# Kernel tuning notes

Hardware: AMD Instinct MI355X
Metric: run time of the kernel (lower is better)

Reference implementation:

```python
import jax, jax.numpy as jnp
import numpy as np

N_NODES = 50000
N_EDGES = 800000
D = 96
DEPTH = 2


def setup_inputs() -> dict:
    key = jax.random.key(0)
    ks = jax.random.split(key, 8)
    scale = 1.0 / np.sqrt(D)
    x = jax.random.normal(ks[0], (N_NODES, D), dtype=jnp.float32)
    W0 = jax.random.normal(ks[1], (DEPTH, D, D), dtype=jnp.float32) * scale
    b0 = jnp.zeros((DEPTH, D), dtype=jnp.float32)
    W1 = jax.random.normal(ks[2], (DEPTH, D, D), dtype=jnp.float32) * scale
    b1 = jnp.zeros((DEPTH, D), dtype=jnp.float32)
    W2 = jax.random.normal(ks[3], (DEPTH, 2 * D, D), dtype=jnp.float32) * (1.0 / np.sqrt(2 * D))
    b2 = jnp.zeros((DEPTH, D), dtype=jnp.float32)
    edge_src = jax.random.randint(ks[4], (N_EDGES,), 0, N_NODES, dtype=jnp.int64 if jax.config.jax_enable_x64 else jnp.int32)
    edge_dst = jnp.sort(jax.random.randint(ks[5], (N_EDGES,), 0, N_NODES, dtype=jnp.int64 if jax.config.jax_enable_x64 else jnp.int32))
    return {"x": x, "W0": W0, "b0": b0, "W1": W1, "b1": b1,
            "W2": W2, "b2": b2, "edge_src": edge_src, "edge_dst": edge_dst}


def reference(x, W0, b0, W1, b1, W2, b2, edge_src, edge_dst):
    # x: [N, D] node features; edge lists define sparse adjacency A (A[dst, src] = 1).
    n = x.shape[0]
    depth = W0.shape[0]
    for i in range(depth):
        h_self = x @ W1[i] + b1[i]                      # [N, D] self transform
        h_nb = x @ W0[i] + b0[i]                        # [N, D] neighbor transform
        # sparse.mm(A, h_nb): sum of h_nb over in-neighbors of each vertex
        agg = jax.ops.segment_sum(h_nb[edge_src], edge_dst, num_segments=n)  # [N, D]
        x = jnp.concatenate([h_self, agg], axis=-1) @ W2[i] + b2[i]          # [N, D]
        # torch.std uses unbiased estimator (ddof=1)
        x = x / jnp.std(x, axis=-1, ddof=1, keepdims=True)
    return x
```

## Files before the change

kernel.cpp:

```cpp
#include <hip/hip_runtime.h>
#include <hip/hip_bf16.h>

typedef __attribute__((ext_vector_type(8))) short short8;
typedef __attribute__((ext_vector_type(16))) float f32x16;

__device__ __forceinline__ float bf2f(unsigned short h){
  union{unsigned u; float f;} c; c.u = ((unsigned)h)<<16; return c.f;
}
__device__ __forceinline__ unsigned short f2bf(float f){
  union{float f; unsigned u;} c; c.f = f;
  return (unsigned short)((c.u + 0x7fffu + ((c.u>>16)&1u))>>16);
}


__global__ void k_wcb(const float* __restrict__ W0, const float* __restrict__ W1,
                      const float* __restrict__ W2, const float* __restrict__ b0,
                      const float* __restrict__ b1, const float* __restrict__ b2,
                      unsigned short* __restrict__ WcF, float* __restrict__ cvec,
                      float* __restrict__ dvec, int depth){
  int b = blockIdx.x, c = threadIdx.x;
  int nwc = depth*192;
  if (b < nwc){
    int i = b/192, k = b%192;
    const float* w  = (k<96) ? (W1 + (size_t)i*96*96 + (size_t)k*96)
                             : (W0 + (size_t)i*96*96 + (size_t)(k-96)*96);
    const float* w2 = W2 + (size_t)i*192*96 + (k<96 ? 0 : 96*96);
    float s0=0.f,s1=0.f,s2=0.f,s3=0.f;
    for (int j=0;j<96;j+=4){
      s0 += w[j]   * w2[(j)*96 + c];
      s1 += w[j+1] * w2[(j+1)*96 + c];
      s2 += w[j+2] * w2[(j+2)*96 + c];
      s3 += w[j+3] * w2[(j+3)*96 + c];
    }
    float s = (s0+s1)+(s2+s3);
    int kt = k>>4, hfk=(k>>3)&1, jj=k&7;
    int t=c>>5, cl=c&31;
    WcF[(size_t)((i*12+kt)*3+t)*512 + (size_t)(hfk*32+cl)*8 + jj] = f2bf(s);
  } else {
    int i = b - nwc;
    const float* w2 = W2 + (size_t)i*192*96;
    float s = b2[i*96+c], d=0.f;
    for (int j=0;j<96;++j){
      s += b1[i*96+j]*w2[j*96+c];
      d += b0[i*96+j]*w2[(96+j)*96+c];
    }
    cvec[i*96+c]=s; dvec[i*96+c]=d;
  }
}

__global__ __launch_bounds__(256) void k_prep(
    const float* __restrict__ x, unsigned short* __restrict__ xb,
    unsigned short* __restrict__ xf, const int* __restrict__ dst, int nE,
    int* __restrict__ rs, int nN, int castBlocks){
  if ((int)blockIdx.x < castBlocks){
    int tid = blockIdx.x*256 + threadIdx.x;
    if (tid >= nN*12) return;
    int n = tid/12, q = tid%12;
    const float4* src = reinterpret_cast<const float4*>(x + (size_t)n*96 + q*8);
    float4 f0 = src[0], f1 = src[1];
    uint4 o;
    o.x = (unsigned)f2bf(f0.x) | ((unsigned)f2bf(f0.y)<<16);
    o.y = (unsigned)f2bf(f0.z) | ((unsigned)f2bf(f0.w)<<16);
    o.z = (unsigned)f2bf(f1.x) | ((unsigned)f2bf(f1.y)<<16);
    o.w = (unsigned)f2bf(f1.z) | ((unsigned)f2bf(f1.w)<<16);
    *reinterpret_cast<uint4*>(xb + (size_t)n*96 + q*8) = o;
    int strip=n>>5, cl=n&31, kt=q>>1, hf=q&1;
    *reinterpret_cast<uint4*>(xf + ((size_t)(strip*6+kt)*64 + hf*32+cl)*8) = o;
  } else {
    int n = ((int)blockIdx.x - castBlocks)*256 + threadIdx.x;
    if (n > nN) return;
    int lo=0, hi=nE;
    while(lo<hi){int mid=(lo+hi)>>1; if(dst[mid]<n) lo=mid+1; else hi=mid;}
    rs[n]=lo;
  }
}

__global__ __launch_bounds__(256) void k_frag(
    const unsigned short* __restrict__ xb, unsigned short* __restrict__ xf, int nN){
  int tid = blockIdx.x*256+threadIdx.x;
  if (tid >= nN*12) return;
  int n=tid/12, q=tid%12;
  uint4 v = *reinterpret_cast<const uint4*>(xb + (size_t)n*96 + q*8);
  int strip=n>>5, cl=n&31, kt=q>>1, hf=q&1;
  *reinterpret_cast<uint4*>(xf + ((size_t)(strip*6+kt)*64 + hf*32+cl)*8) = v;
}

__device__ __forceinline__ void acc8(float* a, uint4 v){
  a[0] += bf2f((unsigned short)(v.x & 0xffffu));
  a[1] += bf2f((unsigned short)(v.x >> 16));
  a[2] += bf2f((unsigned short)(v.y & 0xffffu));
  a[3] += bf2f((unsigned short)(v.y >> 16));
  a[4] += bf2f((unsigned short)(v.z & 0xffffu));
  a[5] += bf2f((unsigned short)(v.z >> 16));
  a[6] += bf2f((unsigned short)(v.w & 0xffffu));
  a[7] += bf2f((unsigned short)(v.w >> 16));
}

__global__ __launch_bounds__(192) void k_agg(
    const unsigned short* __restrict__ xb, const int* __restrict__ esrc,
    const int* __restrict__ rs, unsigned short* __restrict__ xaf,
    int* __restrict__ deg, int nN)
{
  int n = blockIdx.x*16 + threadIdx.y;
  if (n >= nN) return;
  const int q = threadIdx.x;
  const unsigned short* xq = xb + q*8;
  const int e0 = rs[n], e1 = rs[n+1];
  if (q == 0) deg[n] = e1 - e0;

  float a[8] = {0,0,0,0,0,0,0,0};

  int e = e0;
  for (; e+8 <= e1; e += 8){
    int s0 = esrc[e],   s1 = esrc[e+1], s2 = esrc[e+2], s3 = esrc[e+3];
    int s4 = esrc[e+4], s5 = esrc[e+5], s6 = esrc[e+6], s7 = esrc[e+7];
    uint4 v0 = *reinterpret_cast<const uint4*>(xq + (size_t)s0*96);
    uint4 v1 = *reinterpret_cast<const uint4*>(xq + (size_t)s1*96);
    uint4 v2 = *reinterpret_cast<const uint4*>(xq + (size_t)s2*96);
    uint4 v3 = *reinterpret_cast<const uint4*>(xq + (size_t)s3*96);
    uint4 v4 = *reinterpret_cast<const uint4*>(xq + (size_t)s4*96);
    uint4 v5 = *reinterpret_cast<const uint4*>(xq + (size_t)s5*96);
    uint4 v6 = *reinterpret_cast<const uint4*>(xq + (size_t)s6*96);
    uint4 v7 = *reinterpret_cast<const uint4*>(xq + (size_t)s7*96);
    acc8(a, v0); acc8(a, v1); acc8(a, v2); acc8(a, v3);
    acc8(a, v4); acc8(a, v5); acc8(a, v6); acc8(a, v7);
  }
  for (; e+4 <= e1; e += 4){
    int s0 = esrc[e], s1 = esrc[e+1], s2 = esrc[e+2], s3 = esrc[e+3];
    uint4 v0 = *reinterpret_cast<const uint4*>(xq + (size_t)s0*96);
    uint4 v1 = *reinterpret_cast<const uint4*>(xq + (size_t)s1*96);
    uint4 v2 = *reinterpret_cast<const uint4*>(xq + (size_t)s2*96);
    uint4 v3 = *reinterpret_cast<const uint4*>(xq + (size_t)s3*96);
    acc8(a, v0); acc8(a, v1); acc8(a, v2); acc8(a, v3);
  }
  for (; e < e1; ++e){
    int s = esrc[e];
    uint4 v = *reinterpret_cast<const uint4*>(xq + (size_t)s*96);
    acc8(a, v);
  }

  uint4 o;
  o.x = (unsigned)f2bf(a[0]) | ((unsigned)f2bf(a[1]) << 16);
  o.y = (unsigned)f2bf(a[2]) | ((unsigned)f2bf(a[3]) << 16);
  o.z = (unsigned)f2bf(a[4]) | ((unsigned)f2bf(a[5]) << 16);
  o.w = (unsigned)f2bf(a[6]) | ((unsigned)f2bf(a[7]) << 16);
  int strip=n>>5, cl=n&31, kt=q>>1, hf=q&1;
  *reinterpret_cast<uint4*>(xaf + ((size_t)(strip*6+kt)*64 + hf*32+cl)*8) = o;
}

template<int LAST>
__global__ __launch_bounds__(256) void k_gemm(
    const unsigned short* __restrict__ xf, const unsigned short* __restrict__ xaf,
    const unsigned short* __restrict__ WcF, const float* __restrict__ cvec,
    const float* __restrict__ dvec, const int* __restrict__ deg,
    float* __restrict__ outf, unsigned short* __restrict__ outb, int nN)
{
  const int wid = (blockIdx.x<<2) + (threadIdx.x>>6);
  const int nstrips = (nN+31)>>5;
  if (wid >= nstrips) return;
  const int lane = threadIdx.x & 63;
  const int cl = lane & 31;
  const int hf = lane >> 5;
  const int row0 = wid << 5;

  const short8* xfp = reinterpret_cast<const short8*>(xf)  + (size_t)wid*6*64;
  const short8* xap = reinterpret_cast<const short8*>(xaf) + (size_t)wid*6*64;
  const short8* wf  = reinterpret_cast<const short8*>(WcF);

  short8 afr[12];
  #pragma unroll
  for (int kt=0; kt<6; ++kt){ afr[kt] = xfp[kt*64 + lane]; afr[6+kt] = xap[kt*64 + lane]; }

  f32x16 acc[3];
  #pragma unroll
  for (int t=0;t<3;++t){
    #pragma unroll
    for (int i=0;i<16;++i) acc[t][i] = 0.f;
  }

  #pragma unroll
  for (int kt=0; kt<12; ++kt){
    short8 a = afr[kt];
    #pragma unroll
    for (int t=0;t<3;++t){
      short8 b = wf[(kt*3+t)*64 + lane];
      acc[t] = __builtin_amdgcn_mfma_f32_32x32x16_bf16(a, b, acc[t], 0, 0, 0);
    }
  }

  float cv[3], dv[3];
  #pragma unroll
  for (int t=0;t<3;++t){ cv[t] = cvec[t*32+cl]; dv[t] = dvec[t*32+cl]; }

  #pragma unroll
  for (int r=0;r<16;++r){
    const int rl = (r&3) + ((r>>2)<<3) + (hf<<2);
    const int rg = row0 + rl;
    const int rgc = rg < nN ? rg : nN-1;
    const float dgv = (float)deg[rgc];
    float v0 = acc[0][r] + cv[0] + dgv*dv[0];
    float v1 = acc[1][r] + cv[1] + dgv*dv[1];
    float v2 = acc[2][r] + cv[2] + dgv*dv[2];
    float s  = v0+v1+v2;
    float s2 = v0*v0 + v1*v1 + v2*v2;
    #pragma unroll
    for (int m=1;m<32;m<<=1){ s += __shfl_xor(s,m,64); s2 += __shfl_xor(s2,m,64); }
    float var = (s2 - s*s*(1.0f/96.0f)) * (1.0f/95.0f);
    float sc  = 1.0f / sqrtf(var);
    if (rg < nN){
      if (LAST){
        float* o = outf + (size_t)rg*96;
        o[cl] = v0*sc; o[32+cl] = v1*sc; o[64+cl] = v2*sc;
      } else {
        unsigned short* o = outb + (size_t)rg*96;
        o[cl] = f2bf(v0*sc); o[32+cl] = f2bf(v1*sc); o[64+cl] = f2bf(v2*sc);
      }
    }
  }
}

extern "C" void kernel_launch(void* const* d_in, const int* in_sizes, int n_in,
                              void* d_out, int out_size, void* d_ws, size_t ws_size,
                              hipStream_t stream)
{
  const float* x   = (const float*)d_in[0];
  const float* W0  = (const float*)d_in[1];
  const float* b0  = (const float*)d_in[2];
  const float* W1  = (const float*)d_in[3];
  const float* b1  = (const float*)d_in[4];
  const float* W2  = (const float*)d_in[5];
  const float* b2  = (const float*)d_in[6];
  const int* esrc  = (const int*)d_in[7];
  const int* edst  = (const int*)d_in[8];
  const int nN = in_sizes[0] / 96;
  const int nE = in_sizes[7];
  const int depth = in_sizes[1] / (96*96);
  float* out = (float*)d_out;

  const int nstrips = (nN+31)/32;

  char* p = (char*)d_ws;
  auto alloc = [&](size_t bytes)->char*{ char* r = p; p += (bytes + 255) & ~(size_t)255; return r; };
  unsigned short* WcF  = (unsigned short*)alloc((size_t)depth*12*3*512*2);
  float* cvec          = (float*)alloc((size_t)depth*96*4);
  float* dvec          = (float*)alloc((size_t)depth*96*4);
  int* rs              = (int*)alloc((size_t)(nN+1)*4);
  int* deg             = (int*)alloc((size_t)nN*4);
  unsigned short* xb0  = (unsigned short*)alloc((size_t)nN*96*2);
  unsigned short* xb1  = (unsigned short*)alloc((size_t)nN*96*2);
  unsigned short* xf   = (unsigned short*)alloc((size_t)nstrips*3072*2);
  unsigned short* xaf  = (unsigned short*)alloc((size_t)nstrips*3072*2);

  k_wcb<<<dim3(depth*192+depth), dim3(96), 0, stream>>>(W0, W1, W2, b0, b1, b2,
                                                        WcF, cvec, dvec, depth);
  const int castBlocks = (nN*12+255)/256;
  const int rpBlocks   = (nN+1+255)/256;
  k_prep<<<dim3(castBlocks+rpBlocks), dim3(256), 0, stream>>>(x, xb0, xf, edst, nE, rs, nN, castBlocks);

  const int aggGrid  = (nN+15)/16;
  const int gemmGrid = (nstrips+3)/4;
  const int fragGrid = castBlocks;

  unsigned short* cur = xb0;
  unsigned short* nxt = xb1;
  for (int i=0; i<depth; ++i){
    k_agg<<<dim3(aggGrid), dim3(12,16), 0, stream>>>(cur, esrc, rs, xaf, deg, nN);
    if (i == depth-1){
      k_gemm<1><<<dim3(gemmGrid), dim3(256), 0, stream>>>(
          xf, xaf, WcF + (size_t)i*12*3*512, cvec + i*96, dvec + i*96, deg,
          out, (unsigned short*)nullptr, nN);
    } else {
      k_gemm<0><<<dim3(gemmGrid), dim3(256), 0, stream>>>(
          xf, xaf, WcF + (size_t)i*12*3*512, cvec + i*96, dvec + i*96, deg,
          (float*)nullptr, nxt, nN);
      k_frag<<<dim3(fragGrid), dim3(256), 0, stream>>>(nxt, xf, nN);
      unsigned short* t = cur; cur = nxt; nxt = t;
    }
  }
}
```

Measured before the change: 185.3 us.

## Fuse fragment relayout into GEMM epilogue and merge prep kernels into one launch

The weight-combine, bias-fold, cast and row-pointer kernels are merged into a single launch. The weight-combine part now splits its inner reduction across two thread halves and combines them through shared memory. The separate k_frag pass that re-laid out the intermediate activations into MFMA fragment order is removed. The non-last GEMM epilogue now writes that fragment layout directly, alongside the row-major bf16 output. This removes two kernel launches and one full read/write pass over the node features, at the cost of scattered 2-byte stores in the GEMM epilogue. It also overwrites xf in place, which is safe only because each wave reads its own strip before writing it.

Measured after the change: 177.8 us. 1.04x faster.

```diff
diff --git a/kernel.cpp b/kernel.cpp
--- a/kernel.cpp
+++ b/kernel.cpp
@@ -13,49 +13,60 @@
 }
 
 
-__global__ void k_wcb(const float* __restrict__ W0, const float* __restrict__ W1,
-                      const float* __restrict__ W2, const float* __restrict__ b0,
-                      const float* __restrict__ b1, const float* __restrict__ b2,
-                      unsigned short* __restrict__ WcF, float* __restrict__ cvec,
-                      float* __restrict__ dvec, int depth){
-  int b = blockIdx.x, c = threadIdx.x;
-  int nwc = depth*192;
+__global__ __launch_bounds__(256) void k_pre(
+    const float* __restrict__ x,  const float* __restrict__ W0,
+    const float* __restrict__ W1, const float* __restrict__ W2,
+    const float* __restrict__ b0, const float* __restrict__ b1,
+    const float* __restrict__ b2, const int* __restrict__ dst,
+    unsigned short* __restrict__ WcF, float* __restrict__ cvec,
+    float* __restrict__ dvec, unsigned short* __restrict__ xb,
+    unsigned short* __restrict__ xf, int* __restrict__ rs,
+    int nN, int nE, int depth, int castBlocks)
+{
+  const int b = blockIdx.x, tid = threadIdx.x;
+  const int nwc = depth*192;
   if (b < nwc){
+    __shared__ float sm[96];
     int i = b/192, k = b%192;
-    const float* w  = (k<96) ? (W1 + (size_t)i*96*96 + (size_t)k*96)
-                             : (W0 + (size_t)i*96*96 + (size_t)(k-96)*96);
-    const float* w2 = W2 + (size_t)i*192*96 + (k<96 ? 0 : 96*96);
-    float s0=0.f,s1=0.f,s2=0.f,s3=0.f;
-    for (int j=0;j<96;j+=4){
-      s0 += w[j]   * w2[(j)*96 + c];
-      s1 += w[j+1] * w2[(j+1)*96 + c];
-      s2 += w[j+2] * w2[(j+2)*96 + c];
-      s3 += w[j+3] * w2[(j+3)*96 + c];
-    }
-    float s = (s0+s1)+(s2+s3);
-    int kt = k>>4, hfk=(k>>3)&1, jj=k&7;
-    int t=c>>5, cl=c&31;
-    WcF[(size_t)((i*12+kt)*3+t)*512 + (size_t)(hfk*32+cl)*8 + jj] = f2bf(s);
-  } else {
+    float s = 0.f;
+    if (tid < 192){
+      int c = tid % 96, jh = tid / 96;
+      const float* w  = (k<96) ? (W1 + (size_t)i*9216 + (size_t)k*96)
+                               : (W0 + (size_t)i*9216 + (size_t)(k-96)*96);
+      const float* w2 = W2 + (size_t)i*18432 + (k<96 ? 0 : 9216);
+      int j0 = jh*48;
+      float s0=0.f,s1=0.f,s2=0.f,s3=0.f;
+      for (int j=j0;j<j0+48;j+=4){
+        s0 += w[j]   * w2[(j)*96 + c];
+        s1 += w[j+1] * w2[(j+1)*96 + c];
+        s2 += w[j+2] * w2[(j+2)*96 + c];
+        s3 += w[j+3] * w2[(j+3)*96 + c];
+      }
+      s = (s0+s1)+(s2+s3);
+      if (jh==1) sm[c] = s;
+    }
+    __syncthreads();
+    if (tid < 96){
+      float tot = s + sm[tid];
+      int kt=k>>4, hfk=(k>>3)&1, jj=k&7;
+      int t=tid>>5, cl=tid&31;
+      WcF[(size_t)((i*12+kt)*3+t)*512 + (size_t)(hfk*32+cl)*8 + jj] = f2bf(tot);
+    }
+  } else if (b < nwc + depth){
     int i = b - nwc;
-    const float* w2 = W2 + (size_t)i*192*96;
-    float s = b2[i*96+c], d=0.f;
-    for (int j=0;j<96;++j){
-      s += b1[i*96+j]*w2[j*96+c];
-      d += b0[i*96+j]*w2[(96+j)*96+c];
-    }
-    cvec[i*96+c]=s; dvec[i*96+c]=d;
-  }
-}
-
-__global__ __launch_bounds__(256) void k_prep(
-    const float* __restrict__ x, unsigned short* __restrict__ xb,
-    unsigned short* __restrict__ xf, const int* __restrict__ dst, int nE,
-    int* __restrict__ rs, int nN, int castBlocks){
-  if ((int)blockIdx.x < castBlocks){
-    int tid = blockIdx.x*256 + threadIdx.x;
-    if (tid >= nN*12) return;
-    int n = tid/12, q = tid%12;
+    if (tid < 96){
+      const float* w2 = W2 + (size_t)i*18432;
+      float s = b2[i*96+tid], d=0.f;
+      for (int j=0;j<96;++j){
+        s += b1[i*96+j]*w2[j*96+tid];
+        d += b0[i*96+j]*w2[(96+j)*96+tid];
+      }
+      cvec[i*96+tid]=s; dvec[i*96+tid]=d;
+    }
+  } else if (b < nwc + depth + castBlocks){
+    int t2 = (b - nwc - depth)*256 + tid;
+    if (t2 >= nN*12) return;
+    int n = t2/12, q = t2%12;
     const float4* src = reinterpret_cast<const float4*>(x + (size_t)n*96 + q*8);
     float4 f0 = src[0], f1 = src[1];
     uint4 o;
@@ -67,22 +78,12 @@
     int strip=n>>5, cl=n&31, kt=q>>1, hf=q&1;
     *reinterpret_cast<uint4*>(xf + ((size_t)(strip*6+kt)*64 + hf*32+cl)*8) = o;
   } else {
-    int n = ((int)blockIdx.x - castBlocks)*256 + threadIdx.x;
+    int n = (b - nwc - depth - castBlocks)*256 + tid;
     if (n > nN) return;
     int lo=0, hi=nE;
     while(lo<hi){int mid=(lo+hi)>>1; if(dst[mid]<n) lo=mid+1; else hi=mid;}
     rs[n]=lo;
   }
-}
-
-__global__ __launch_bounds__(256) void k_frag(
-    const unsigned short* __restrict__ xb, unsigned short* __restrict__ xf, int nN){
-  int tid = blockIdx.x*256+threadIdx.x;
-  if (tid >= nN*12) return;
-  int n=tid/12, q=tid%12;
-  uint4 v = *reinterpret_cast<const uint4*>(xb + (size_t)n*96 + q*8);
-  int strip=n>>5, cl=n&31, kt=q>>1, hf=q&1;
-  *reinterpret_cast<uint4*>(xf + ((size_t)(strip*6+kt)*64 + hf*32+cl)*8) = v;
 }
 
 __device__ __forceinline__ void acc8(float* a, uint4 v){
@@ -153,7 +154,8 @@
     const unsigned short* __restrict__ xf, const unsigned short* __restrict__ xaf,
     const unsigned short* __restrict__ WcF, const float* __restrict__ cvec,
     const float* __restrict__ dvec, const int* __restrict__ deg,
-    float* __restrict__ outf, unsigned short* __restrict__ outb, int nN)
+    float* __restrict__ outf, unsigned short* __restrict__ outb,
+    unsigned short* __restrict__ xfo, int nN)
 {
   const int wid = (blockIdx.x<<2) + (threadIdx.x>>6);
   const int nstrips = (nN+31)>>5;
@@ -191,6 +193,10 @@
   float cv[3], dv[3];
   #pragma unroll
   for (int t=0;t<3;++t){ cv[t] = cvec[t*32+cl]; dv[t] = dvec[t*32+cl]; }
+
+  const int jj  = cl & 7;
+  const int hfd = (cl >> 3) & 1;
+  const int ktb = cl >> 4;
 
   #pragma unroll
   for (int r=0;r<16;++r){
@@ -212,8 +218,13 @@
         float* o = outf + (size_t)rg*96;
         o[cl] = v0*sc; o[32+cl] = v1*sc; o[64+cl] = v2*sc;
       } else {
+        unsigned short h0 = f2bf(v0*sc), h1 = f2bf(v1*sc), h2 = f2bf(v2*sc);
         unsigned short* o = outb + (size_t)rg*96;
-        o[cl] = f2bf(v0*sc); o[32+cl] = f2bf(v1*sc); o[64+cl] = f2bf(v2*sc);
+        o[cl] = h0; o[32+cl] = h1; o[64+cl] = h2;
+        size_t base = (size_t)wid*3072 + (size_t)(hfd*32 + rl)*8 + jj;
+        xfo[base + (size_t)(ktb  )*512] = h0;
+        xfo[base + (size_t)(ktb+2)*512] = h1;
+        xfo[base + (size_t)(ktb+4)*512] = h2;
       }
     }
   }
@@ -251,15 +262,15 @@
   unsigned short* xf   = (unsigned short*)alloc((size_t)nstrips*3072*2);
   unsigned short* xaf  = (unsigned short*)alloc((size_t)nstrips*3072*2);
 
-  k_wcb<<<dim3(depth*192+depth), dim3(96), 0, stream>>>(W0, W1, W2, b0, b1, b2,
-                                                        WcF, cvec, dvec, depth);
   const int castBlocks = (nN*12+255)/256;
   const int rpBlocks   = (nN+1+255)/256;
-  k_prep<<<dim3(castBlocks+rpBlocks), dim3(256), 0, stream>>>(x, xb0, xf, edst, nE, rs, nN, castBlocks);
+  const int preGrid    = depth*192 + depth + castBlocks + rpBlocks;
+  k_pre<<<dim3(preGrid), dim3(256), 0, stream>>>(
+      x, W0, W1, W2, b0, b1, b2, edst, WcF, cvec, dvec, xb0, xf, rs,
+      nN, nE, depth, castBlocks);
 
   const int aggGrid  = (nN+15)/16;
   const int gemmGrid = (nstrips+3)/4;
-  const int fragGrid = castBlocks;
 
   unsigned short* cur = xb0;
   unsigned short* nxt = xb1;
@@ -268,12 +279,11 @@
     if (i == depth-1){
       k_gemm<1><<<dim3(gemmGrid), dim3(256), 0, stream>>>(
           xf, xaf, WcF + (size_t)i*12*3*512, cvec + i*96, dvec + i*96, deg,
-          out, (unsigned short*)nullptr, nN);
+          out, (unsigned short*)nullptr, (unsigned short*)nullptr, nN);
     } else {
       k_gemm<0><<<dim3(gemmGrid), dim3(256), 0, stream>>>(
           xf, xaf, WcF + (size_t)i*12*3*512, cvec + i*96, dvec + i*96, deg,
-          (float*)nullptr, nxt, nN);
-      k_frag<<<dim3(fragGrid), dim3(256), 0, stream>>>(nxt, xf, nN);
+          (float*)nullptr, nxt, xf, nN);
       unsigned short* t = cur; cur = nxt; nxt = t;
     }
   }
```
